# Performance work log

Measured on AMD Instinct MI355X. Metric: run time of the kernel, lower is better.

## Reference

```python
import jax, jax.numpy as jnp
import numpy as np

EMBED_DIM = 1024
N_HEADS = 16
HEAD_DIM = EMBED_DIM // N_HEADS
B, S = 2, 2048


def setup_inputs() -> dict:
    key = jax.random.key(0)
    ks = jax.random.split(key, 8)
    scale = 1.0 / np.sqrt(EMBED_DIM)
    return {
        "key": jax.random.normal(ks[0], (B, S, EMBED_DIM), jnp.float32),
        "query": jax.random.normal(ks[1], (B, S, EMBED_DIM), jnp.float32),
        "value": jax.random.normal(ks[2], (B, S, EMBED_DIM), jnp.float32),
        # nn.Linear weights stored [out_features, in_features], applied as x @ W.T
        "Wq": jax.random.normal(ks[3], (EMBED_DIM, EMBED_DIM), jnp.float32) * scale,
        "Wk": jax.random.normal(ks[4], (EMBED_DIM, EMBED_DIM), jnp.float32) * scale,
        "Wv": jax.random.normal(ks[5], (EMBED_DIM, EMBED_DIM), jnp.float32) * scale,
        "Wo": jax.random.normal(ks[6], (EMBED_DIM, EMBED_DIM), jnp.float32) * scale,
        "bo": jax.random.normal(ks[7], (EMBED_DIM,), jnp.float32) * scale,
    }


def reference(key, query, value, Wq, Wk, Wv, Wo, bo) -> jnp.ndarray:
    b = key.shape[0]
    # project and split heads: [B, S, E] -> [B, H, S, D]
    def split_heads(x):
        return x.reshape(b, -1, N_HEADS, HEAD_DIM).transpose(0, 2, 1, 3)
    q = split_heads(query @ Wq.T)
    k = split_heads(key @ Wk.T)
    v = split_heads(value @ Wv.T)
    scores = jnp.einsum("bhqd,bhkd->bhqk", q, k) / np.sqrt(HEAD_DIM)
    attn = jax.nn.softmax(scores, axis=-1)
    ctx = jnp.einsum("bhqk,bhkd->bhqd", attn, v)  # [B, H, S, D]
    ctx = ctx.transpose(0, 2, 1, 3).reshape(b, -1, EMBED_DIM)
    return ctx @ Wo.T + bo
```

## Files before the change

### kernel.cpp

```cpp
#include <hip/hip_runtime.h>

typedef unsigned short u16;
typedef __bf16 bf8 __attribute__((ext_vector_type(8)));
typedef __bf16 bf2 __attribute__((ext_vector_type(2)));
typedef float f4 __attribute__((ext_vector_type(4)));

typedef __attribute__((address_space(1))) const unsigned int gas_u32;
typedef __attribute__((address_space(3))) unsigned int las_u32;
#define ASYNC16(g, l) __builtin_amdgcn_global_load_lds((gas_u32*)(g), (las_u32*)(l), 16, 0, 0)

__device__ __forceinline__ u16 f2bf(float f) {
    union { float f; unsigned int u; } v; v.f = f;
    return (u16)((v.u + 0x7fffu + ((v.u >> 16) & 1u)) >> 16);
}

__device__ __forceinline__ unsigned pkbf(float lo, float hi) {
    union { bf2 v; unsigned u; } t;
    t.v[0] = (__bf16)lo;
    t.v[1] = (__bf16)hi;
    return t.u;
}

__device__ __forceinline__ float fexp2(float x) {
#if __has_builtin(__builtin_amdgcn_exp2f)
  return __builtin_amdgcn_exp2f(x);
#else
  return __expf(x * 0.69314718056f);
#endif
}

__global__ __launch_bounds__(256) void cvt_all(
    const float* __restrict__ k_, const float* __restrict__ q_, const float* __restrict__ v_,
    const float* __restrict__ wq, const float* __restrict__ wk, const float* __restrict__ wv,
    const float* __restrict__ wo, u16* __restrict__ ws) {
  size_t e = ((size_t)blockIdx.x * 256 + threadIdx.x) * 8;
  const float* src;
  if      (e <  4194304) src = k_ + e;
  else if (e <  8388608) src = q_ + (e - 4194304);
  else if (e < 12582912) src = v_ + (e - 8388608);
  else if (e < 13631488) src = wq + (e - 12582912);
  else if (e < 14680064) src = wk + (e - 13631488);
  else if (e < 15728640) src = wv + (e - 14680064);
  else                   src = wo + (e - 15728640);
  float4 f0 = ((const float4*)src)[0];
  float4 f1 = ((const float4*)src)[1];
  uint4 o;
  o.x = (unsigned)f2bf(f0.x) | ((unsigned)f2bf(f0.y) << 16);
  o.y = (unsigned)f2bf(f0.z) | ((unsigned)f2bf(f0.w) << 16);
  o.z = (unsigned)f2bf(f1.x) | ((unsigned)f2bf(f1.y) << 16);
  o.w = (unsigned)f2bf(f1.z) | ((unsigned)f2bf(f1.w) << 16);
  *(uint4*)(ws + e) = o;
}

template<int BM, bool FINAL>
__device__ __forceinline__ void gemm_tile(const u16* __restrict__ A, const u16* __restrict__ Bm,
                                          u16* __restrict__ Cb, float* __restrict__ Cf,
                                          const float* __restrict__ bias, float scale,
                                          int bm, int bn, int ldc) {
  __shared__ u16 As[BM*64];
  __shared__ u16 Bs[128*64];
  const int tid = threadIdx.x;
  const int wave = tid >> 6, lane = tid & 63;
  const int wm = wave >> 1, wn = wave & 1;
  const int quad = lane >> 4, l16 = lane & 15;
  const int MI = BM / 32;

  f4 acc[MI][4];
  const f4 zz = {0.f, 0.f, 0.f, 0.f};
  #pragma unroll
  for (int i = 0; i < MI; i++)
    #pragma unroll
    for (int j = 0; j < 4; j++) acc[i][j] = zz;

  const int kr = tid >> 3;
  const int cs = (tid & 7) ^ (kr & 7);
  const u16* ga = A  + (size_t)(bm*BM  + kr)*1024 + cs*8;
  const u16* gb = Bm + (size_t)(bn*128 + kr)*1024 + cs*8;
  u16* la = As + tid*8;
  u16* lb = Bs + tid*8;

  for (int kt = 0; kt < 1024; kt += 64) {
    #pragma unroll
    for (int p = 0; p < BM/32; p++) ASYNC16(ga + (size_t)(p*32)*1024 + kt, la + p*2048);
    #pragma unroll
    for (int p = 0; p < 4; p++)     ASYNC16(gb + (size_t)(p*32)*1024 + kt, lb + p*2048);
    __syncthreads();
    #pragma unroll
    for (int kk = 0; kk < 2; kk++) {
      bf8 af[MI];
      #pragma unroll
      for (int mi = 0; mi < MI; mi++)
        af[mi] = *(const bf8*)(As + (wm*(BM/2) + mi*16 + l16)*64 + (((kk*4 + quad) ^ (l16 & 7))*8));
      #pragma unroll
      for (int ni = 0; ni < 4; ni++) {
        bf8 bfr = *(const bf8*)(Bs + (wn*64 + ni*16 + l16)*64 + (((kk*4 + quad) ^ (l16 & 7))*8));
        #pragma unroll
        for (int mi = 0; mi < MI; mi++)
          acc[mi][ni] = __builtin_amdgcn_mfma_f32_16x16x32_bf16(af[mi], bfr, acc[mi][ni], 0, 0, 0);
      }
    }
    __syncthreads();
  }

  #pragma unroll
  for (int mi = 0; mi < MI; mi++)
    #pragma unroll
    for (int ni = 0; ni < 4; ni++) {
      const int col = bn*128 + wn*64 + ni*16 + l16;
      #pragma unroll
      for (int r = 0; r < 4; r++) {
        const int row = bm*BM + wm*(BM/2) + mi*16 + quad*4 + r;
        if (FINAL) Cf[(size_t)row*ldc + col] = acc[mi][ni][r] + bias[col];
        else       Cb[(size_t)row*ldc + col] = f2bf(acc[mi][ni][r] * scale);
      }
    }
}

#define QSCALE 0.180336880f

__global__ __launch_bounds__(256, 3) void gemm_qkv(
    const u16* __restrict__ xq, const u16* __restrict__ xk, const u16* __restrict__ xv,
    const u16* __restrict__ wq, const u16* __restrict__ wk, const u16* __restrict__ wv,
    u16* __restrict__ Qo, u16* __restrict__ Ko, u16* __restrict__ Vto) {
  if (blockIdx.z == 0)
    gemm_tile<128,false>(xq, wq, Qo, nullptr, nullptr, QSCALE, blockIdx.x, blockIdx.y, 1024);
  else if (blockIdx.z == 1)
    gemm_tile<128,false>(xk, wk, Ko, nullptr, nullptr, 1.0f, blockIdx.x, blockIdx.y, 1024);
  else
    gemm_tile<128,false>(wv, xv, Vto, nullptr, nullptr, 1.0f, blockIdx.y, blockIdx.x, 4096);
}

__global__ __launch_bounds__(256, 2) void gemm_out(
    const u16* __restrict__ ctx, const u16* __restrict__ wo,
    const float* __restrict__ bias, float* __restrict__ out) {
  gemm_tile<64,true>(ctx, wo, nullptr, out, bias, 1.0f, blockIdx.x, blockIdx.y, 1024);
}

__global__ __launch_bounds__(256, 3) void flash_attn(
    const u16* __restrict__ Qg, const u16* __restrict__ Kg,
    const u16* __restrict__ Vtg, u16* __restrict__ ctx) {
  __shared__ uint4 smem4[2560];
  u16* Ks = (u16*)smem4;
  u16* Vt = (u16*)smem4 + 8192;
  u16* Pt = (u16*)smem4 + 16384;
  float* Of = (float*)smem4;
  float* Lf = (float*)smem4 + 2*64*68;

  const int tid = threadIdx.x;
  const int wave = tid >> 6, lane = tid & 63;
  const int quad = lane >> 4, l16 = lane & 15;
  const int wq = wave >> 1, wk = wave & 1;
  const int h = blockIdx.x, qt = blockIdx.y, b = blockIdx.z;
  u16* Ptw = Pt + wave*1024;

  bf8 qf[2][2];
  {
    const u16* qp = Qg + (size_t)(b*2048 + qt*64 + wq*32)*1024 + h*64;
    #pragma unroll
    for (int qs = 0; qs < 2; qs++)
      #pragma unroll
      for (int kc = 0; kc < 2; kc++)
        qf[qs][kc] = *(const bf8*)(qp + (size_t)(qs*16 + l16)*1024 + kc*32 + quad*8);
  }

  const f4 zz = {0.f, 0.f, 0.f, 0.f};
  f4 ot[4][2];
  float lrow[2] = {0.f, 0.f};
  #pragma unroll
  for (int ds = 0; ds < 4; ds++)
    #pragma unroll
    for (int qs = 0; qs < 2; qs++) ot[ds][qs] = zz;

  const int kr = tid >> 3;
  const u16* kga = Kg + (size_t)(b*2048 + kr)*1024 + h*64 + ((tid & 7) ^ (kr & 7))*8;
  const int vd = tid >> 4;
  const u16* vga = Vtg + (size_t)(h*64 + vd)*4096 + b*2048 + (((tid & 15) ^ vd))*8;
  u16* kld = Ks + tid*8;
  u16* vld = Vt + tid*8;

  for (int kv0 = 0; kv0 < 2048; kv0 += 128) {
    __syncthreads();
    #pragma unroll
    for (int p = 0; p < 4; p++) ASYNC16(kga + (size_t)(kv0 + p*32)*1024, kld + p*2048);
    #pragma unroll
    for (int p = 0; p < 4; p++) ASYNC16(vga + (size_t)(p*16)*4096 + kv0, vld + p*2048);
    __syncthreads();

    #pragma unroll
    for (int kb = 0; kb < 2; kb++) {
      f4 st[2][2];
      #pragma unroll
      for (int ks = 0; ks < 2; ks++)
        #pragma unroll
        for (int qs = 0; qs < 2; qs++) st[ks][qs] = zz;
      #pragma unroll
      for (int ks = 0; ks < 2; ks++) {
        const int key = wk*64 + kb*32 + ks*16 + l16;
        #pragma unroll
        for (int kc = 0; kc < 2; kc++) {
          bf8 kf = *(const bf8*)(Ks + key*64 + (((kc*4 + quad) ^ (l16 & 7))*8));
          #pragma unroll
          for (int qs = 0; qs < 2; qs++)
            st[ks][qs] = __builtin_amdgcn_mfma_f32_16x16x32_bf16(kf, qf[qs][kc], st[ks][qs], 0, 0, 0);
        }
      }
      #pragma unroll
      for (int ks = 0; ks < 2; ks++)
        #pragma unroll
        for (int qs = 0; qs < 2; qs++) {
          float p0 = fexp2(st[ks][qs][0]), p1 = fexp2(st[ks][qs][1]);
          float p2 = fexp2(st[ks][qs][2]), p3 = fexp2(st[ks][qs][3]);
          lrow[qs] += (p0 + p1) + (p2 + p3);
          uint2 w;
          w.x = pkbf(p0, p1);
          w.y = pkbf(p2, p3);
          *(uint2*)(Ptw + (qs*16 + l16)*32 + (((ks*4 + quad) ^ (l16 & 7))*4)) = w;
        }
      bf8 pf[2];
      #pragma unroll
      for (int qs = 0; qs < 2; qs++) {
        uint2 a = *(const uint2*)(Ptw + (qs*16 + l16)*32 + (((quad*2 + 0) ^ (l16 & 7))*4));
        uint2 c = *(const uint2*)(Ptw + (qs*16 + l16)*32 + (((quad*2 + 1) ^ (l16 & 7))*4));
        union { uint4 u; bf8 v; } pu;
        pu.u.x = a.x; pu.u.y = a.y; pu.u.z = c.x; pu.u.w = c.y;
        pf[qs] = pu.v;
      }
      #pragma unroll
      for (int ds = 0; ds < 4; ds++) {
        const int d = ds*16 + l16;
        bf8 vf = *(const bf8*)(Vt + d*128 + (((wk*8 + kb*4 + quad) ^ l16)*8));
        #pragma unroll
        for (int qs = 0; qs < 2; qs++)
          ot[ds][qs] = __builtin_amdgcn_mfma_f32_16x16x32_bf16(vf, pf[qs], ot[ds][qs], 0, 0, 0);
      }
    }
  }

  __syncthreads();
  #pragma unroll
  for (int qs = 0; qs < 2; qs++) {
    lrow[qs] += __shfl_xor(lrow[qs], 16);
    lrow[qs] += __shfl_xor(lrow[qs], 32);
  }
  float* Ofw = Of + wk*(64*68);
  #pragma unroll
  for (int ds = 0; ds < 4; ds++)
    #pragma unroll
    for (int qs = 0; qs < 2; qs++)
      #pragma unroll
      for (int r = 0; r < 4; r++)
        Ofw[(wq*32 + qs*16 + l16)*68 + ds*16 + quad*4 + r] = ot[ds][qs][r];
  if (quad == 0) {
    Lf[wk*64 + wq*32 + l16]      = lrow[0];
    Lf[wk*64 + wq*32 + 16 + l16] = lrow[1];
  }
  __syncthreads();
  {
    const int qr = tid >> 2, dp = (tid & 3)*16;
    const float inv = 1.f / (Lf[qr] + Lf[64 + qr]);
    const float* o0 = Of + qr*68 + dp;
    const float* o1 = o0 + 64*68;
    unsigned ow[8];
    #pragma unroll
    for (int i = 0; i < 8; i++)
      ow[i] = pkbf((o0[2*i] + o1[2*i]) * inv, (o0[2*i+1] + o1[2*i+1]) * inv);
    u16* cp = ctx + (size_t)(b*2048 + qt*64 + qr)*1024 + h*64 + dp;
    *(uint4*)cp       = *(uint4*)&ow[0];
    *(uint4*)(cp + 8) = *(uint4*)&ow[4];
  }
}

extern "C" void kernel_launch(void* const* d_in, const int* in_sizes, int n_in,
                              void* d_out, int out_size, void* d_ws, size_t ws_size,
                              hipStream_t stream) {
  const float* key_  = (const float*)d_in[0];
  const float* query = (const float*)d_in[1];
  const float* value = (const float*)d_in[2];
  const float* Wq = (const float*)d_in[3];
  const float* Wk = (const float*)d_in[4];
  const float* Wv = (const float*)d_in[5];
  const float* Wo = (const float*)d_in[6];
  const float* bo = (const float*)d_in[7];
  float* out = (float*)d_out;

  u16* ws  = (u16*)d_ws;
  u16* xkb = ws;
  u16* xqb = ws + 4194304;
  u16* xvb = ws + 8388608;
  u16* Wqb = ws + 12582912;
  u16* Wkb = ws + 13631488;
  u16* Wvb = ws + 14680064;
  u16* Wob = ws + 15728640;
  u16* Qb  = ws + 16777216;
  u16* Kb  = ws + 20971520;
  u16* Vtb = ws + 25165824;
  u16* Cb  = ws + 29360128;

  cvt_all<<<8192, 256, 0, stream>>>(key_, query, value, Wq, Wk, Wv, Wo, ws);
  gemm_qkv<<<dim3(32, 8, 3), 256, 0, stream>>>(xqb, xkb, xvb, Wqb, Wkb, Wvb, Qb, Kb, Vtb);
  flash_attn<<<dim3(16, 32, 2), 256, 0, stream>>>(Qb, Kb, Vtb, Cb);
  gemm_out<<<dim3(64, 8), 256, 0, stream>>>(Cb, Wob, bo, out);
}
```

Baseline: 201.9 us.

## Permute key rows so softmax P feeds PV MFMA directly from registers

Reorders which key rows each lane loads for the QK^T MFMA so that the score accumulator layout matches the B-operand layout needed by the PV MFMA. This removes the per-wave LDS staging buffer for P and its write/read round trip. The smaller shared memory footprint allows raising launch bounds occupancy to 4 blocks per CU. It depends on the permuted key ordering matching the V column ordering used in the PV product.

```diff
diff --git a/kernel.cpp b/kernel.cpp
--- a/kernel.cpp
+++ b/kernel.cpp
@@ -136,13 +136,12 @@
   gemm_tile<64,true>(ctx, wo, nullptr, out, bias, 1.0f, blockIdx.x, blockIdx.y, 1024);
 }
 
-__global__ __launch_bounds__(256, 3) void flash_attn(
+__global__ __launch_bounds__(256, 4) void flash_attn(
     const u16* __restrict__ Qg, const u16* __restrict__ Kg,
     const u16* __restrict__ Vtg, u16* __restrict__ ctx) {
-  __shared__ uint4 smem4[2560];
+  __shared__ uint4 smem4[2208];
   u16* Ks = (u16*)smem4;
   u16* Vt = (u16*)smem4 + 8192;
-  u16* Pt = (u16*)smem4 + 16384;
   float* Of = (float*)smem4;
   float* Lf = (float*)smem4 + 2*64*68;
 
@@ -151,7 +150,6 @@
   const int quad = lane >> 4, l16 = lane & 15;
   const int wq = wave >> 1, wk = wave & 1;
   const int h = blockIdx.x, qt = blockIdx.y, b = blockIdx.z;
-  u16* Ptw = Pt + wave*1024;
 
   bf8 qf[2][2];
   {
@@ -178,6 +176,9 @@
   u16* kld = Ks + tid*8;
   u16* vld = Vt + tid*8;
 
+  const int prow0 = ((l16 >> 2) << 3) + (l16 & 3);
+  const int prow1 = prow0 + 4;
+
   for (int kv0 = 0; kv0 < 2048; kv0 += 128) {
     __syncthreads();
     #pragma unroll
@@ -190,39 +191,33 @@
     for (int kb = 0; kb < 2; kb++) {
       f4 st[2][2];
       #pragma unroll
-      for (int ks = 0; ks < 2; ks++)
-        #pragma unroll
-        for (int qs = 0; qs < 2; qs++) st[ks][qs] = zz;
-      #pragma unroll
-      for (int ks = 0; ks < 2; ks++) {
-        const int key = wk*64 + kb*32 + ks*16 + l16;
+      for (int f = 0; f < 2; f++)
+        #pragma unroll
+        for (int qs = 0; qs < 2; qs++) st[f][qs] = zz;
+      #pragma unroll
+      for (int f = 0; f < 2; f++) {
+        const int row = wk*64 + kb*32 + (f ? prow1 : prow0);
         #pragma unroll
         for (int kc = 0; kc < 2; kc++) {
-          bf8 kf = *(const bf8*)(Ks + key*64 + (((kc*4 + quad) ^ (l16 & 7))*8));
+          bf8 kf = *(const bf8*)(Ks + row*64 + (((kc*4 + quad) ^ (row & 7))*8));
           #pragma unroll
           for (int qs = 0; qs < 2; qs++)
-            st[ks][qs] = __builtin_amdgcn_mfma_f32_16x16x32_bf16(kf, qf[qs][kc], st[ks][qs], 0, 0, 0);
+            st[f][qs] = __builtin_amdgcn_mfma_f32_16x16x32_bf16(kf, qf[qs][kc], st[f][qs], 0, 0, 0);
         }
       }
-      #pragma unroll
-      for (int ks = 0; ks < 2; ks++)
-        #pragma unroll
-        for (int qs = 0; qs < 2; qs++) {
-          float p0 = fexp2(st[ks][qs][0]), p1 = fexp2(st[ks][qs][1]);
-          float p2 = fexp2(st[ks][qs][2]), p3 = fexp2(st[ks][qs][3]);
-          lrow[qs] += (p0 + p1) + (p2 + p3);
-          uint2 w;
-          w.x = pkbf(p0, p1);
-          w.y = pkbf(p2, p3);
-          *(uint2*)(Ptw + (qs*16 + l16)*32 + (((ks*4 + quad) ^ (l16 & 7))*4)) = w;
-        }
       bf8 pf[2];
       #pragma unroll
       for (int qs = 0; qs < 2; qs++) {
-        uint2 a = *(const uint2*)(Ptw + (qs*16 + l16)*32 + (((quad*2 + 0) ^ (l16 & 7))*4));
-        uint2 c = *(const uint2*)(Ptw + (qs*16 + l16)*32 + (((quad*2 + 1) ^ (l16 & 7))*4));
+        float p0 = fexp2(st[0][qs][0]), p1 = fexp2(st[0][qs][1]);
+        float p2 = fexp2(st[0][qs][2]), p3 = fexp2(st[0][qs][3]);
+        float p4 = fexp2(st[1][qs][0]), p5 = fexp2(st[1][qs][1]);
+        float p6 = fexp2(st[1][qs][2]), p7 = fexp2(st[1][qs][3]);
+        lrow[qs] += ((p0 + p1) + (p2 + p3)) + ((p4 + p5) + (p6 + p7));
         union { uint4 u; bf8 v; } pu;
-        pu.u.x = a.x; pu.u.y = a.y; pu.u.z = c.x; pu.u.w = c.y;
+        pu.u.x = pkbf(p0, p1);
+        pu.u.y = pkbf(p2, p3);
+        pu.u.z = pkbf(p4, p5);
+        pu.u.w = pkbf(p6, p7);
         pf[qs] = pu.v;
       }
       #pragma unroll
```

Result: no change. 203.5 us (+0.8%).
